# Performance work log

Measured on AMD Instinct MI355X. Metric: run time of the kernel, lower is better.

Reference implementation:

```python
import jax, jax.numpy as jnp
import numpy as np

B, N, D, R = 32, 1024, 1152, 4


def setup_inputs() -> dict:
    key = jax.random.key(0)
    ks = jax.random.split(key, 9)
    s = 1.0 / np.sqrt(D)
    return {
        "x": jax.random.normal(ks[0], (B, N, D), dtype=jnp.float32),
        "Wq": jax.random.uniform(ks[1], (D, D), jnp.float32, -s, s),
        "bq": jax.random.uniform(ks[2], (D,), jnp.float32, -s, s),
        "Wk": jax.random.uniform(ks[3], (D, D), jnp.float32, -s, s),
        "bk": jax.random.uniform(ks[4], (D,), jnp.float32, -s, s),
        "Wv": jax.random.uniform(ks[5], (D, D), jnp.float32, -s, s),
        "bv": jax.random.uniform(ks[6], (D,), jnp.float32, -s, s),
        "Wo": jax.random.uniform(ks[7], (D, D), jnp.float32, -s, s),
        "bo": jax.random.uniform(ks[8], (D,), jnp.float32, -s, s),
        "r": R,
    }


def _merge(t, r):
    # VisionTokenMerger: non-overlapping window-mean over r consecutive tokens.
    b, n, d = t.shape
    merged = t.reshape(b, n // r, r, d).mean(axis=2)  # [B, N/r, D]
    return merged, r  # num_patches_per_token is the scalar window size


def reference(x, Wq, bq, Wk, bk, Wv, bv, Wo, bo, r):
    Q = x @ Wq.T + bq
    K = x @ Wk.T + bk
    V = x @ Wv.T + bv
    K_m, npt = _merge(K, r)            # [B, M, D], M = N/r
    V_m, _ = _merge(V, r)
    scale = 1.0 / jnp.sqrt(jnp.float32(Q.shape[-1]))
    scores = jnp.einsum('bnd,bmd->bnm', Q, K_m) * scale
    scores = scores + jnp.log(jnp.float32(npt))  # log-count additive bias
    w = jax.nn.softmax(scores, axis=-1)
    out = jnp.einsum('bnm,bmd->bnd', w, V_m)
    return out @ Wo.T + bo
```

## Files before the change

### kernel.cpp

```cpp
#include <hip/hip_runtime.h>
#include <hip/hip_bf16.h>


typedef __bf16 bf16;
typedef __attribute__((ext_vector_type(8))) __bf16 bf16x8;
typedef __attribute__((ext_vector_type(4))) __bf16 bf16x4;
typedef __attribute__((ext_vector_type(4))) float f32x4;

#define GAS __attribute__((address_space(1)))
#define LAS __attribute__((address_space(3)))

__device__ __forceinline__ void async_copy16(const void* g, void* s) {
    __builtin_amdgcn_global_load_lds((GAS unsigned int*)g, (LAS unsigned int*)s, 16, 0, 0);
}

template <typename OutT, bool HAS_BIAS>
__global__ __launch_bounds__(256) void gemm_bt(
    const bf16* __restrict__ A, const bf16* __restrict__ B,
    const float* __restrict__ bias, OutT* __restrict__ C,
    int N, int K, int lda, int ldb, int ldc, float scale,
    long sAb, long sBb, long sCb) {
    __shared__ __align__(16) bf16 As[128 * 32];
    __shared__ __align__(16) bf16 Bs[128 * 32];
    const int tid  = threadIdx.x;
    const int wave = tid >> 6;
    const int lane = tid & 63;
    const int quad = lane >> 4;
    const int l16  = lane & 15;
    const int wM   = (wave >> 1) * 64;
    const int wN   = (wave & 1) * 64;

    int bx = blockIdx.x, by = blockIdx.y;
    const int nbx = gridDim.x, nby = gridDim.y;
    if (((nby & 7) == 0) && (nbx % 9 == 0)) {
        int lid = by * nbx + bx;
        int xcd = lid & 7;
        int s   = lid >> 3;
        int Pn  = nby >> 3;
        int gsz = 9 * Pn;
        int g   = s / gsz;
        int rem = s - g * gsz;
        int p   = rem / 9;
        by = p * 8 + xcd;
        bx = g * 9 + (rem - p * 9);
    }

    const long zb = blockIdx.z;
    A += zb * sAb;
    B += zb * sBb;
    C += zb * sCb;

    const int rowBase = by * 128;
    const int colBase = bx * 128;

    const int g0 = wave * 64 + lane;
    const int r0 = g0 >> 2;
    const int c0 = (g0 & 3) * 8;
    const bf16* a0 = A + (long)(rowBase + r0) * lda + c0;
    const bf16* a1 = A + (long)(rowBase + 64 + r0) * lda + c0;
    const bf16* b0 = B + (long)(colBase + r0) * ldb + c0;
    const bf16* b1 = B + (long)(colBase + 64 + r0) * ldb + c0;
    char* lA0 = (char*)As + wave * 1024;
    char* lA1 = (char*)As + 4096 + wave * 1024;
    char* lB0 = (char*)Bs + wave * 1024;
    char* lB1 = (char*)Bs + 4096 + wave * 1024;

    f32x4 acc[4][4] = {};

    const int kt = K >> 5;
    for (int k = 0; k < kt; ++k) {
        __syncthreads();
        async_copy16(a0, lA0);
        async_copy16(a1, lA1);
        async_copy16(b0, lB0);
        async_copy16(b1, lB1);
        a0 += 32; a1 += 32; b0 += 32; b1 += 32;
        __syncthreads();
        bf16x8 af[4], bfv[4];
#pragma unroll
        for (int t = 0; t < 4; ++t) {
            af[t]  = *(const bf16x8*)(As + (wM + t * 16 + l16) * 32 + quad * 8);
            bfv[t] = *(const bf16x8*)(Bs + (wN + t * 16 + l16) * 32 + quad * 8);
        }
#pragma unroll
        for (int mt = 0; mt < 4; ++mt)
#pragma unroll
            for (int nt = 0; nt < 4; ++nt)
                acc[mt][nt] = __builtin_amdgcn_mfma_f32_16x16x32_bf16(
                    af[mt], bfv[nt], acc[mt][nt], 0, 0, 0);
    }

#pragma unroll
    for (int mt = 0; mt < 4; ++mt) {
        const int row = rowBase + wM + mt * 16 + quad * 4;
#pragma unroll
        for (int nt = 0; nt < 4; ++nt) {
            const int col = colBase + wN + nt * 16 + l16;
            const float bv = HAS_BIAS ? bias[col] : 0.0f;
#pragma unroll
            for (int r = 0; r < 4; ++r) {
                float v = acc[mt][nt][r] * scale + bv;
                C[(long)(row + r) * ldc + col] = (OutT)v;
            }
        }
    }
}

__global__ __launch_bounds__(512) void scores_softmax_k(
    const bf16* __restrict__ X, const bf16* __restrict__ UVW,
    const float* __restrict__ cvec, bf16* __restrict__ P) {
    __shared__ __align__(16) bf16 As[128 * 32];
    __shared__ __align__(16) bf16 Bs[256 * 32];
    __shared__ float red[128][4];
    __shared__ float red2[128][4];
    const int tid  = threadIdx.x;
    const int wave = tid >> 6;
    const int lane = tid & 63;
    const int quad = lane >> 4;
    const int l16  = lane & 15;
    const int wM   = (wave >> 2) * 64;
    const int wN   = (wave & 3) * 64;
    const int wc   = wave & 3;

    int bx = blockIdx.x, by = blockIdx.y;
    {
        int lid = by * 8 + bx;
        int xcd = lid & 7;
        int s   = lid >> 3;
        by = (s >> 3) * 8 + xcd;
        bx = s & 7;
    }
    const long b = by;
    const bf16* A = X + (b * 1024 + (long)bx * 128) * 1152;
    const bf16* B = UVW + b * 256 * 2304;

    const int ra = tid >> 2, ca = (tid & 3) * 8;
    const bf16* a0 = A + (long)ra * 1152 + ca;
    const bf16* b0 = B + (long)ra * 2304 + ca;
    const bf16* b1 = B + (long)(128 + ra) * 2304 + ca;
    char* lA  = (char*)As + wave * 1024;
    char* lB0 = (char*)Bs + wave * 1024;
    char* lB1 = (char*)Bs + 8192 + wave * 1024;

    f32x4 acc[4][4] = {};
#pragma unroll 1
    for (int k = 0; k < 36; ++k) {
        __syncthreads();
        async_copy16(a0, lA);
        async_copy16(b0, lB0);
        async_copy16(b1, lB1);
        a0 += 32; b0 += 32; b1 += 32;
        __syncthreads();
        bf16x8 af[4], bfv[4];
#pragma unroll
        for (int t = 0; t < 4; ++t) {
            af[t]  = *(const bf16x8*)(As + (wM + t * 16 + l16) * 32 + quad * 8);
            bfv[t] = *(const bf16x8*)(Bs + (wN + t * 16 + l16) * 32 + quad * 8);
        }
#pragma unroll
        for (int mt = 0; mt < 4; ++mt)
#pragma unroll
            for (int nt = 0; nt < 4; ++nt)
                acc[mt][nt] = __builtin_amdgcn_mfma_f32_16x16x32_bf16(
                    af[mt], bfv[nt], acc[mt][nt], 0, 0, 0);
    }

    float cv[4];
#pragma unroll
    for (int nt = 0; nt < 4; ++nt) cv[nt] = cvec[b * 256 + wN + nt * 16 + l16];
#pragma unroll
    for (int mt = 0; mt < 4; ++mt)
#pragma unroll
        for (int nt = 0; nt < 4; ++nt)
#pragma unroll
            for (int r = 0; r < 4; ++r) acc[mt][nt][r] += cv[nt];

    const float scale = 0.029462782549439484f;

#pragma unroll
    for (int mt = 0; mt < 4; ++mt)
#pragma unroll
        for (int r = 0; r < 4; ++r) {
            float pm = fmaxf(fmaxf(acc[mt][0][r], acc[mt][1][r]),
                             fmaxf(acc[mt][2][r], acc[mt][3][r]));
#pragma unroll
            for (int off = 1; off <= 8; off <<= 1) pm = fmaxf(pm, __shfl_xor(pm, off));
            if (l16 == 0) red[wM + mt * 16 + quad * 4 + r][wc] = pm;
        }
    __syncthreads();
#pragma unroll
    for (int mt = 0; mt < 4; ++mt)
#pragma unroll
        for (int r = 0; r < 4; ++r) {
            const int R = wM + mt * 16 + quad * 4 + r;
            float4 q = *(const float4*)red[R];
            float m = fmaxf(fmaxf(q.x, q.y), fmaxf(q.z, q.w));
            float ps = 0.0f;
#pragma unroll
            for (int nt = 0; nt < 4; ++nt) {
                float e = __expf((acc[mt][nt][r] - m) * scale);
                acc[mt][nt][r] = e;
                ps += e;
            }
#pragma unroll
            for (int off = 1; off <= 8; off <<= 1) ps += __shfl_xor(ps, off);
            if (l16 == 0) red2[R][wc] = ps;
        }
    __syncthreads();
#pragma unroll
    for (int mt = 0; mt < 4; ++mt)
#pragma unroll
        for (int r = 0; r < 4; ++r) {
            const int R = wM + mt * 16 + quad * 4 + r;
            float4 q = *(const float4*)red2[R];
            float inv = 1.0f / (q.x + q.y + q.z + q.w);
            const long gr = b * 1024 + (long)bx * 128 + R;
#pragma unroll
            for (int nt = 0; nt < 4; ++nt)
                P[gr * 256 + wN + nt * 16 + l16] = (bf16)(acc[mt][nt][r] * inv);
        }
}

__global__ void cvt_wT_k(const float* __restrict__ Wq, const float* __restrict__ Wk,
                         const float* __restrict__ Wv, bf16* __restrict__ dst) {
    __shared__ bf16 t[64][66];
    const int z = blockIdx.z;
    const float* src = z == 0 ? Wq : z == 1 ? Wk : Wv;
    bf16* d = dst + (long)(z == 0 ? 0 : z == 1 ? 2 : 3) * 1327104;
    const int r0 = blockIdx.y * 64, c0 = blockIdx.x * 64;
    const int tid = threadIdx.x;
    {
        int row = tid >> 4;
        int col4 = (tid & 15) * 4;
#pragma unroll
        for (int p = 0; p < 4; ++p) {
            int r = row + p * 16;
            float4 v = *(const float4*)(src + (long)(r0 + r) * 1152 + c0 + col4);
            t[col4 + 0][r] = (bf16)v.x;
            t[col4 + 1][r] = (bf16)v.y;
            t[col4 + 2][r] = (bf16)v.z;
            t[col4 + 3][r] = (bf16)v.w;
        }
    }
    __syncthreads();
    {
        int orow = tid >> 2;
        int oc = (tid & 3) * 16;
        bf16x8 a, b2;
#pragma unroll
        for (int j = 0; j < 8; ++j) { a[j] = t[orow][oc + j]; b2[j] = t[orow][oc + 8 + j]; }
        bf16* o = d + (long)(c0 + orow) * 1152 + r0 + oc;
        *(bf16x8*)o = a;
        *(bf16x8*)(o + 8) = b2;
    }
}

__global__ void cvt_w_plain_k(const float* __restrict__ Wo, bf16* __restrict__ dst) {
    int i = blockIdx.x * 256 + threadIdx.x;
    float4 v = ((const float4*)Wo)[i];
    bf16x4 o = {(bf16)v.x, (bf16)v.y, (bf16)v.z, (bf16)v.w};
    ((bf16x4*)(dst + 1327104))[i] = o;
}

__global__ void cvt_merge_x_k(const float* __restrict__ x, bf16* __restrict__ xb,
                              bf16* __restrict__ xm) {
    int i = blockIdx.x * 256 + threadIdx.x;
    int w = i / 288;
    int c4 = i - w * 288;
    const float4* p = (const float4*)(x + (long)w * 4608) + c4;
    float4 a = p[0], b = p[288], c = p[576], d = p[864];
    bf16x4 oa = {(bf16)a.x, (bf16)a.y, (bf16)a.z, (bf16)a.w};
    bf16x4 ob = {(bf16)b.x, (bf16)b.y, (bf16)b.z, (bf16)b.w};
    bf16x4 oc = {(bf16)c.x, (bf16)c.y, (bf16)c.z, (bf16)c.w};
    bf16x4 od = {(bf16)d.x, (bf16)d.y, (bf16)d.z, (bf16)d.w};
    bf16* base = xb + (long)w * 4608 + c4 * 4;
    *(bf16x4*)(base)        = oa;
    *(bf16x4*)(base + 1152) = ob;
    *(bf16x4*)(base + 2304) = oc;
    *(bf16x4*)(base + 3456) = od;
    float4 s;
    s.x = (a.x + b.x + c.x + d.x) * 0.25f;
    s.y = (a.y + b.y + c.y + d.y) * 0.25f;
    s.z = (a.z + b.z + c.z + d.z) * 0.25f;
    s.w = (a.w + b.w + c.w + d.w) * 0.25f;
    bf16x4 o = {(bf16)s.x, (bf16)s.y, (bf16)s.z, (bf16)s.w};
    *(bf16x4*)(xm + (long)w * 1152 + c4 * 4) = o;
}

__global__ void rowdot_k(const bf16* __restrict__ M, const float* __restrict__ v,
                         float* __restrict__ out, float* __restrict__ z) {
    const int row = blockIdx.x * 4 + (threadIdx.x >> 6);
    const int lane = threadIdx.x & 63;
    const bf16* mr = M + (long)row * 1152;
    float acc = 0.0f;
#pragma unroll
    for (int j = 0; j < 18; ++j)
        acc += (float)mr[j * 64 + lane] * v[j * 64 + lane];
#pragma unroll
    for (int off = 32; off; off >>= 1) acc += __shfl_xor(acc, off, 64);
    if (lane == 0) {
        out[row] = acc;
        if (z) z[row] = 0.0f;
    }
}

__global__ void transpose_vm_k(const bf16* __restrict__ UVW, bf16* __restrict__ VT) {
    __shared__ bf16 t[64][65];
    const int tid = threadIdx.x;
    const int b = blockIdx.z;
    const int d0 = blockIdx.x * 64, m0 = blockIdx.y * 64;
#pragma unroll
    for (int p = 0; p < 2; ++p) {
        int r = (tid >> 3) + p * 32;
        int c = (tid & 7) * 8;
        bf16x8 v = *(const bf16x8*)(UVW + (long)(b * 256 + m0 + r) * 2304 + 1152 + d0 + c);
#pragma unroll
        for (int j = 0; j < 8; ++j) t[c + j][r] = v[j];
    }
    __syncthreads();
#pragma unroll
    for (int p = 0; p < 2; ++p) {
        int r = (tid >> 3) + p * 32;
        int c = (tid & 7) * 8;
        bf16x8 o;
#pragma unroll
        for (int j = 0; j < 8; ++j) o[j] = t[r][c + j];
        *(bf16x8*)(VT + (long)b * 294912 + (long)(d0 + r) * 256 + m0 + c) = o;
    }
}

extern "C" void kernel_launch(void* const* d_in, const int* in_sizes, int n_in,
                              void* d_out, int out_size, void* d_ws, size_t ws_size,
                              hipStream_t stream) {
    const float* x  = (const float*)d_in[0];
    const float* Wq = (const float*)d_in[1];
    const float* bq = (const float*)d_in[2];
    const float* Wk = (const float*)d_in[3];
    const float* bk = (const float*)d_in[4];  (void)bk;
    const float* Wv = (const float*)d_in[5];
    const float* bv = (const float*)d_in[6];
    const float* Wo = (const float*)d_in[7];
    const float* bo = (const float*)d_in[8];
    float* out = (float*)d_out;
    char* ws = (char*)d_ws;

    bf16* WT4    = (bf16*)(ws);
    bf16* WkT_b  = WT4 + 2 * 1327104;
    bf16* Wo_b   = WT4 + 1 * 1327104;
    bf16* WQK2   = (bf16*)(ws + 10616832);
    float* biasUV = (float*)(ws + 15925248);
    float* vk     = (float*)(ws + 15934464);
    float* cvec   = (float*)(ws + 15939072);
    bf16* xm_b   = (bf16*)(ws + 15971840);
    bf16* UVW    = (bf16*)(ws + 34846208);
    bf16* VWT    = (bf16*)(ws + 72594944);
    bf16* P_b    = (bf16*)(ws + 91469312);

    bf16* x_b = (bf16*)d_out;

    cvt_wT_k<<<dim3(18, 18, 3), 256, 0, stream>>>(Wq, Wk, Wv, WT4);
    cvt_w_plain_k<<<1296, 256, 0, stream>>>(Wo, WT4);
    cvt_merge_x_k<<<9216, 256, 0, stream>>>(x, x_b, xm_b);

    gemm_bt<bf16, false><<<dim3(9, 9, 2), 256, 0, stream>>>(
        WT4, WT4 + 2 * 1327104, nullptr, WQK2,
        1152, 1152, 1152, 1152, 1152, 1.0f, 1327104, 1327104, 1327104);

    rowdot_k<<<288, 256, 0, stream>>>(WkT_b, bq, vk, biasUV);
    rowdot_k<<<288, 256, 0, stream>>>(Wo_b, bv, biasUV + 1152, nullptr);

    gemm_bt<bf16, true><<<dim3(18, 64, 1), 256, 0, stream>>>(
        xm_b, WQK2, biasUV, UVW, 2304, 1152, 1152, 1152, 2304, 1.0f, 0, 0, 0);

    rowdot_k<<<2048, 256, 0, stream>>>(xm_b, vk, cvec, nullptr);

    transpose_vm_k<<<dim3(18, 4, 32), 256, 0, stream>>>(UVW, VWT);

    scores_softmax_k<<<dim3(8, 32), 512, 0, stream>>>(x_b, UVW, cvec, P_b);

    gemm_bt<float, true><<<dim3(9, 8, 32), 256, 0, stream>>>(
        P_b, VWT, bo, out, 1152, 256, 256, 256, 1152, 1.0f,
        1024L * 256, 1152L * 256, 1024L * 1152);
}
```

Measured before the change: 504.3 us.

## Double-buffer LDS tiles in GEMM and scores kernels to overlap loads with MFMA

Both the generic bf16 GEMM and the fused scores/softmax kernel now keep two LDS buffers per operand. Each iteration issues the async global-to-LDS copy for the next K-slice before running the MFMAs on the current slice. This also drops one of the two barriers per iteration. The aim is to hide global load latency behind matrix math, at the cost of twice the LDS footprint, which may reduce occupancy. Correctness relies on the barrier waiting for outstanding global_load_lds operations.

```diff
diff --git a/kernel.cpp b/kernel.cpp
--- a/kernel.cpp
+++ b/kernel.cpp
@@ -20,8 +20,8 @@
     const float* __restrict__ bias, OutT* __restrict__ C,
     int N, int K, int lda, int ldb, int ldc, float scale,
     long sAb, long sBb, long sCb) {
-    __shared__ __align__(16) bf16 As[128 * 32];
-    __shared__ __align__(16) bf16 Bs[128 * 32];
+    __shared__ __align__(16) bf16 As[2][128 * 32];
+    __shared__ __align__(16) bf16 Bs[2][128 * 32];
     const int tid  = threadIdx.x;
     const int wave = tid >> 6;
     const int lane = tid & 63;
@@ -60,27 +60,36 @@
     const bf16* a1 = A + (long)(rowBase + 64 + r0) * lda + c0;
     const bf16* b0 = B + (long)(colBase + r0) * ldb + c0;
     const bf16* b1 = B + (long)(colBase + 64 + r0) * ldb + c0;
-    char* lA0 = (char*)As + wave * 1024;
-    char* lA1 = (char*)As + 4096 + wave * 1024;
-    char* lB0 = (char*)Bs + wave * 1024;
-    char* lB1 = (char*)Bs + 4096 + wave * 1024;
+    char* lA = (char*)As + wave * 1024;
+    char* lB = (char*)Bs + wave * 1024;
 
     f32x4 acc[4][4] = {};
 
     const int kt = K >> 5;
+    async_copy16(a0, lA);
+    async_copy16(a1, lA + 4096);
+    async_copy16(b0, lB);
+    async_copy16(b1, lB + 4096);
+    a0 += 32; a1 += 32; b0 += 32; b1 += 32;
+    int cur = 0;
     for (int k = 0; k < kt; ++k) {
         __syncthreads();
-        async_copy16(a0, lA0);
-        async_copy16(a1, lA1);
-        async_copy16(b0, lB0);
-        async_copy16(b1, lB1);
-        a0 += 32; a1 += 32; b0 += 32; b1 += 32;
-        __syncthreads();
+        if (k + 1 < kt) {
+            char* nA = lA + ((cur ^ 1) << 13);
+            char* nB = lB + ((cur ^ 1) << 13);
+            async_copy16(a0, nA);
+            async_copy16(a1, nA + 4096);
+            async_copy16(b0, nB);
+            async_copy16(b1, nB + 4096);
+            a0 += 32; a1 += 32; b0 += 32; b1 += 32;
+        }
+        const bf16* Ab = &As[cur][0];
+        const bf16* Bb = &Bs[cur][0];
         bf16x8 af[4], bfv[4];
 #pragma unroll
         for (int t = 0; t < 4; ++t) {
-            af[t]  = *(const bf16x8*)(As + (wM + t * 16 + l16) * 32 + quad * 8);
-            bfv[t] = *(const bf16x8*)(Bs + (wN + t * 16 + l16) * 32 + quad * 8);
+            af[t]  = *(const bf16x8*)(Ab + (wM + t * 16 + l16) * 32 + quad * 8);
+            bfv[t] = *(const bf16x8*)(Bb + (wN + t * 16 + l16) * 32 + quad * 8);
         }
 #pragma unroll
         for (int mt = 0; mt < 4; ++mt)
@@ -88,6 +97,7 @@
             for (int nt = 0; nt < 4; ++nt)
                 acc[mt][nt] = __builtin_amdgcn_mfma_f32_16x16x32_bf16(
                     af[mt], bfv[nt], acc[mt][nt], 0, 0, 0);
+        cur ^= 1;
     }
 
 #pragma unroll
@@ -109,8 +119,8 @@
 __global__ __launch_bounds__(512) void scores_softmax_k(
     const bf16* __restrict__ X, const bf16* __restrict__ UVW,
     const float* __restrict__ cvec, bf16* __restrict__ P) {
-    __shared__ __align__(16) bf16 As[128 * 32];
-    __shared__ __align__(16) bf16 Bs[256 * 32];
+    __shared__ __align__(16) bf16 As[2][128 * 32];
+    __shared__ __align__(16) bf16 Bs[2][256 * 32];
     __shared__ float red[128][4];
     __shared__ float red2[128][4];
     const int tid  = threadIdx.x;
@@ -138,24 +148,33 @@
     const bf16* a0 = A + (long)ra * 1152 + ca;
     const bf16* b0 = B + (long)ra * 2304 + ca;
     const bf16* b1 = B + (long)(128 + ra) * 2304 + ca;
-    char* lA  = (char*)As + wave * 1024;
-    char* lB0 = (char*)Bs + wave * 1024;
-    char* lB1 = (char*)Bs + 8192 + wave * 1024;
+    char* lA = (char*)As + wave * 1024;
+    char* lB = (char*)Bs + wave * 1024;
 
     f32x4 acc[4][4] = {};
+    async_copy16(a0, lA);
+    async_copy16(b0, lB);
+    async_copy16(b1, lB + 8192);
+    a0 += 32; b0 += 32; b1 += 32;
+    int cur = 0;
 #pragma unroll 1
     for (int k = 0; k < 36; ++k) {
         __syncthreads();
-        async_copy16(a0, lA);
-        async_copy16(b0, lB0);
-        async_copy16(b1, lB1);
-        a0 += 32; b0 += 32; b1 += 32;
-        __syncthreads();
+        if (k < 35) {
+            char* nA = lA + ((cur ^ 1) << 13);
+            char* nB = lB + ((cur ^ 1) << 14);
+            async_copy16(a0, nA);
+            async_copy16(b0, nB);
+            async_copy16(b1, nB + 8192);
+            a0 += 32; b0 += 32; b1 += 32;
+        }
+        const bf16* Ab = &As[cur][0];
+        const bf16* Bb = &Bs[cur][0];
         bf16x8 af[4], bfv[4];
 #pragma unroll
         for (int t = 0; t < 4; ++t) {
-            af[t]  = *(const bf16x8*)(As + (wM + t * 16 + l16) * 32 + quad * 8);
-            bfv[t] = *(const bf16x8*)(Bs + (wN + t * 16 + l16) * 32 + quad * 8);
+            af[t]  = *(const bf16x8*)(Ab + (wM + t * 16 + l16) * 32 + quad * 8);
+            bfv[t] = *(const bf16x8*)(Bb + (wN + t * 16 + l16) * 32 + quad * 8);
         }
 #pragma unroll
         for (int mt = 0; mt < 4; ++mt)
@@ -163,6 +182,7 @@
             for (int nt = 0; nt < 4; ++nt)
                 acc[mt][nt] = __builtin_amdgcn_mfma_f32_16x16x32_bf16(
                     af[mt], bfv[nt], acc[mt][nt], 0, 0, 0);
+        cur ^= 1;
     }
 
     float cv[4];
```

Measured after the change: 493.4 us. -2.2%, faster.

## Multi-stage pipeline LDS async loads in GEMM and scores kernels

Applied to the files above, without the earlier changes.

Replaces the single-buffered load/sync/compute loop in both the generic GEMM and the fused scores-softmax kernel with a 3-stage and 4-stage ring of LDS buffers. Loads for future K-tiles are issued before computing the current tile, and explicit vmcnt waits plus a single barrier per iteration replace the two __syncthreads. The aim is to hide global-memory latency behind MFMA work. The cost is higher LDS usage, which may reduce occupancy: the scores kernel goes to roughly 100KB+ of LDS. The design also relies on correct hand-placed waitcnt values.

```diff
diff --git a/kernel.cpp b/kernel.cpp
--- a/kernel.cpp
+++ b/kernel.cpp
@@ -9,6 +9,10 @@
 
 #define GAS __attribute__((address_space(1)))
 #define LAS __attribute__((address_space(3)))
+
+#define WAITVM(N) asm volatile("s_waitcnt vmcnt(" #N ")" ::: "memory")
+#define WAITLGKM0 asm volatile("s_waitcnt lgkmcnt(0)" ::: "memory")
+#define BAR() __builtin_amdgcn_s_barrier()
 
 __device__ __forceinline__ void async_copy16(const void* g, void* s) {
     __builtin_amdgcn_global_load_lds((GAS unsigned int*)g, (LAS unsigned int*)s, 16, 0, 0);
@@ -20,8 +24,8 @@
     const float* __restrict__ bias, OutT* __restrict__ C,
     int N, int K, int lda, int ldb, int ldc, float scale,
     long sAb, long sBb, long sCb) {
-    __shared__ __align__(16) bf16 As[128 * 32];
-    __shared__ __align__(16) bf16 Bs[128 * 32];
+    __shared__ __align__(16) bf16 As[3][128 * 32];
+    __shared__ __align__(16) bf16 Bs[3][128 * 32];
     const int tid  = threadIdx.x;
     const int wave = tid >> 6;
     const int lane = tid & 63;
@@ -60,27 +64,29 @@
     const bf16* a1 = A + (long)(rowBase + 64 + r0) * lda + c0;
     const bf16* b0 = B + (long)(colBase + r0) * ldb + c0;
     const bf16* b1 = B + (long)(colBase + 64 + r0) * ldb + c0;
-    char* lA0 = (char*)As + wave * 1024;
-    char* lA1 = (char*)As + 4096 + wave * 1024;
-    char* lB0 = (char*)Bs + wave * 1024;
-    char* lB1 = (char*)Bs + 4096 + wave * 1024;
+    char* lA = (char*)As + wave * 1024;
+    char* lB = (char*)Bs + wave * 1024;
 
     f32x4 acc[4][4] = {};
-
     const int kt = K >> 5;
-    for (int k = 0; k < kt; ++k) {
-        __syncthreads();
-        async_copy16(a0, lA0);
-        async_copy16(a1, lA1);
-        async_copy16(b0, lB0);
-        async_copy16(b1, lB1);
+
+    auto stage = [&](int s) {
+        char* dA = lA + s * 8192;
+        char* dB = lB + s * 8192;
+        async_copy16(a0, dA);
+        async_copy16(a1, dA + 4096);
+        async_copy16(b0, dB);
+        async_copy16(b1, dB + 4096);
         a0 += 32; a1 += 32; b0 += 32; b1 += 32;
-        __syncthreads();
+    };
+    auto compute = [&](int s) {
+        const bf16* Ab = As[s];
+        const bf16* Bb = Bs[s];
         bf16x8 af[4], bfv[4];
 #pragma unroll
         for (int t = 0; t < 4; ++t) {
-            af[t]  = *(const bf16x8*)(As + (wM + t * 16 + l16) * 32 + quad * 8);
-            bfv[t] = *(const bf16x8*)(Bs + (wN + t * 16 + l16) * 32 + quad * 8);
+            af[t]  = *(const bf16x8*)(Ab + (wM + t * 16 + l16) * 32 + quad * 8);
+            bfv[t] = *(const bf16x8*)(Bb + (wN + t * 16 + l16) * 32 + quad * 8);
         }
 #pragma unroll
         for (int mt = 0; mt < 4; ++mt)
@@ -88,7 +94,23 @@
             for (int nt = 0; nt < 4; ++nt)
                 acc[mt][nt] = __builtin_amdgcn_mfma_f32_16x16x32_bf16(
                     af[mt], bfv[nt], acc[mt][nt], 0, 0, 0);
-    }
+    };
+
+    stage(0); stage(1);
+    int rd = 0, st = 2;
+#pragma unroll 1
+    for (int k = 0; k < kt - 2; ++k) {
+        WAITVM(4);
+        WAITLGKM0;
+        BAR();
+        stage(st);
+        compute(rd);
+        rd = rd == 2 ? 0 : rd + 1;
+        st = st == 2 ? 0 : st + 1;
+    }
+    WAITVM(4); WAITLGKM0; BAR(); compute(rd);
+    rd = rd == 2 ? 0 : rd + 1;
+    WAITVM(0); WAITLGKM0; BAR(); compute(rd);
 
 #pragma unroll
     for (int mt = 0; mt < 4; ++mt) {
@@ -109,8 +131,8 @@
 __global__ __launch_bounds__(512) void scores_softmax_k(
     const bf16* __restrict__ X, const bf16* __restrict__ UVW,
     const float* __restrict__ cvec, bf16* __restrict__ P) {
-    __shared__ __align__(16) bf16 As[128 * 32];
-    __shared__ __align__(16) bf16 Bs[256 * 32];
+    __shared__ __align__(16) bf16 As[4][128 * 32];
+    __shared__ __align__(16) bf16 Bs[4][256 * 32];
     __shared__ float red[128][4];
     __shared__ float red2[128][4];
     const int tid  = threadIdx.x;
@@ -138,24 +160,27 @@
     const bf16* a0 = A + (long)ra * 1152 + ca;
     const bf16* b0 = B + (long)ra * 2304 + ca;
     const bf16* b1 = B + (long)(128 + ra) * 2304 + ca;
-    char* lA  = (char*)As + wave * 1024;
-    char* lB0 = (char*)Bs + wave * 1024;
-    char* lB1 = (char*)Bs + 8192 + wave * 1024;
+    char* lA = (char*)As + wave * 1024;
+    char* lB = (char*)Bs + wave * 1024;
 
     f32x4 acc[4][4] = {};
-#pragma unroll 1
-    for (int k = 0; k < 36; ++k) {
-        __syncthreads();
-        async_copy16(a0, lA);
-        async_copy16(b0, lB0);
-        async_copy16(b1, lB1);
+
+    auto stage = [&](int s) {
+        char* dA = lA + s * 8192;
+        char* dB = lB + s * 16384;
+        async_copy16(a0, dA);
+        async_copy16(b0, dB);
+        async_copy16(b1, dB + 8192);
         a0 += 32; b0 += 32; b1 += 32;
-        __syncthreads();
+    };
+    auto compute = [&](int s) {
+        const bf16* Ab = As[s];
+        const bf16* Bb = Bs[s];
         bf16x8 af[4], bfv[4];
 #pragma unroll
         for (int t = 0; t < 4; ++t) {
-            af[t]  = *(const bf16x8*)(As + (wM + t * 16 + l16) * 32 + quad * 8);
-            bfv[t] = *(const bf16x8*)(Bs + (wN + t * 16 + l16) * 32 + quad * 8);
+            af[t]  = *(const bf16x8*)(Ab + (wM + t * 16 + l16) * 32 + quad * 8);
+            bfv[t] = *(const bf16x8*)(Bb + (wN + t * 16 + l16) * 32 + quad * 8);
         }
 #pragma unroll
         for (int mt = 0; mt < 4; ++mt)
@@ -163,7 +188,23 @@
             for (int nt = 0; nt < 4; ++nt)
                 acc[mt][nt] = __builtin_amdgcn_mfma_f32_16x16x32_bf16(
                     af[mt], bfv[nt], acc[mt][nt], 0, 0, 0);
-    }
+    };
+
+    stage(0); stage(1); stage(2);
+    int rd = 0, st = 3;
+#pragma unroll 1
+    for (int k = 0; k < 33; ++k) {
+        WAITVM(6);
+        WAITLGKM0;
+        BAR();
+        stage(st);
+        compute(rd);
+        rd = (rd + 1) & 3;
+        st = (st + 1) & 3;
+    }
+    WAITVM(6); WAITLGKM0; BAR(); compute(rd); rd = (rd + 1) & 3;
+    WAITVM(3); WAITLGKM0; BAR(); compute(rd); rd = (rd + 1) & 3;
+    WAITVM(0); WAITLGKM0; BAR(); compute(rd);
 
     float cv[4];
 #pragma unroll
```

New measurement: 498.9 us. No clear change (-1.1%).
